# Optimization experiments

Hardware: AMD Instinct MI355X
Metric: run time of the kernel (lower is better)

## Reference

```python
import jax, jax.numpy as jnp
import numpy as np

N = 50000      # particles (nodes)
E = 300000     # contacts (directed edges), avg degree 6
H = 128        # hidden_features
L = 6          # num_hidden_layers
GF = 12        # graph (global) feature dim: domain(3)+t(1)+x_global(4)+domain_next(3)+t_next(1)
NG = 1         # number of graphs in batch
SP, SV, SW = 1e-3, 1e-3, 1e-2   # scale_position, scale_velocity, scale_angular_velocity
IN_EMB = GF + 1 + 6              # 19 : r + v + globals
IN_MSG = 2 * H + 3 + 6 + 2 + GF  # 279: h_i,h_j,dpos,dv,r_i,r_j,globals
IN_UPD = 2 * H + GF              # 268: h, aggregated message, globals


def _lin_params(key, fan_in, fan_out):
    k1, k2 = jax.random.split(key)
    s = 1.0 / np.sqrt(fan_in)
    W = jax.random.uniform(k1, (fan_in, fan_out), jnp.float32, -s, s)
    b = jax.random.uniform(k2, (fan_out,), jnp.float32, -s, s)
    return W, b


def setup_inputs() -> dict:
    key = jax.random.key(0)
    ks = jax.random.split(key, 40)
    inp = {}
    inp['v'] = jax.random.normal(ks[0], (N, 6), jnp.float32) * 0.01
    inp['pos'] = jax.random.uniform(ks[1], (N, 3), jnp.float32)
    inp['r'] = jax.random.uniform(ks[2], (N, 1), jnp.float32) * 0.05 + 0.01
    inp['domain'] = jnp.ones((3,), jnp.float32)
    inp['t'] = jnp.full((1,), 0.5, jnp.float32)
    inp['x_global'] = jax.random.normal(ks[3], (4,), jnp.float32)
    inp['domain_next'] = jnp.ones((3,), jnp.float32)
    inp['t_next'] = jnp.full((1,), 0.6, jnp.float32)
    inp['edge_index'] = jax.random.randint(ks[4], (2, E), 0, N, jnp.int32)
    inp['batch'] = jnp.zeros((N,), jnp.int32)
    inp['emb_W1'], inp['emb_b1'] = _lin_params(ks[5], IN_EMB, H)
    inp['emb_W2'], inp['emb_b2'] = _lin_params(ks[6], H, H)
    mw1, mb1, mw2, mb2, uw1, ub1, uw2, ub2 = ([] for _ in range(8))
    for l in range(L):
        W, b = _lin_params(ks[7 + l], IN_MSG, H); mw1.append(W); mb1.append(b)
        W, b = _lin_params(ks[13 + l], H, H);     mw2.append(W); mb2.append(b)
        W, b = _lin_params(ks[19 + l], IN_UPD, H); uw1.append(W); ub1.append(b)
        W, b = _lin_params(ks[25 + l], H, H);     uw2.append(W); ub2.append(b)
    inp['msg_W1'] = jnp.stack(mw1); inp['msg_b1'] = jnp.stack(mb1)
    inp['msg_W2'] = jnp.stack(mw2); inp['msg_b2'] = jnp.stack(mb2)
    inp['upd_W1'] = jnp.stack(uw1); inp['upd_b1'] = jnp.stack(ub1)
    inp['upd_W2'] = jnp.stack(uw2); inp['upd_b2'] = jnp.stack(ub2)
    inp['out_W1'], inp['out_b1'] = _lin_params(ks[31], H, H)
    inp['out_W2'], inp['out_b2'] = _lin_params(ks[32], H, 9)
    inp['mac_W1'], inp['mac_b1'] = _lin_params(ks[33], H, H)
    inp['mac_W2'], inp['mac_b2'] = _lin_params(ks[34], H, 3)
    return inp


def _instance_norm(h, batch):
    # per-graph, per-channel normalization over nodes (PyG InstanceNorm, affine=False)
    cnt = jax.ops.segment_sum(jnp.ones((h.shape[0],), h.dtype), batch, NG)[:, None]
    mean = jax.ops.segment_sum(h, batch, NG) / cnt
    d = h - mean[batch]
    var = jax.ops.segment_sum(d * d, batch, NG) / cnt
    return d / jnp.sqrt(var[batch] + 1e-5)


def reference(v, pos, r, domain, t, x_global, domain_next, t_next, edge_index, batch,
              emb_W1, emb_b1, emb_W2, emb_b2,
              msg_W1, msg_b1, msg_W2, msg_b2,
              upd_W1, upd_b1, upd_W2, upd_b2,
              out_W1, out_b1, out_W2, out_b2,
              mac_W1, mac_b1, mac_W2, mac_b2):
    gf = jnp.concatenate((domain, t, x_global, domain_next, t_next))   # [12]
    gfN = jnp.broadcast_to(gf, (v.shape[0], gf.shape[0]))
    node_features = jnp.concatenate((pos, v), axis=1)                  # [N,9]
    feat = jnp.concatenate((r, v, gfN), axis=1)                        # [N,19]
    h = jax.nn.relu(jax.nn.relu(feat @ emb_W1 + emb_b1) @ emb_W2 + emb_b2)
    src, dst = edge_index[0], edge_index[1]
    ones_e = jnp.ones((src.shape[0],), h.dtype)
    deg = jnp.maximum(jax.ops.segment_sum(ones_e, dst, v.shape[0]), 1.0)[:, None]
    gfE = jnp.broadcast_to(gf, (src.shape[0], gf.shape[0]))
    for l in range(L):
        dpos = pos[dst] - pos[src]
        dpos = dpos - domain * jnp.round(dpos / domain)                # periodic minimum image
        m_in = jnp.concatenate((h[dst], h[src], dpos, v[dst] - v[src], r[dst], r[src], gfE), axis=1)
        m = jax.nn.relu(jax.nn.relu(m_in @ msg_W1[l] + msg_b1[l]) @ msg_W2[l] + msg_b2[l])
        agg = jax.ops.segment_sum(m, dst, v.shape[0]) / deg            # mean aggregation
        u_in = jnp.concatenate((h, agg, gfN), axis=1)
        upd = jax.nn.relu(u_in @ upd_W1[l] + upd_b1[l]) @ upd_W2[l] + upd_b2[l]
        h = _instance_norm(h + upd, batch)                             # residual + InstanceNorm
    out = jax.nn.relu(h @ out_W1 + out_b1) @ out_W2 + out_b2           # [N,9]
    scaled = jnp.concatenate((SP * out[:, :3], SV * out[:, 3:6], SW * out[:, 6:]), axis=1)
    pred = scaled + node_features
    pred_x = jnp.remainder(pred[:, :3], domain_next)
    pred_v = pred[:, 3:]
    cnt = jax.ops.segment_sum(jnp.ones((h.shape[0],), h.dtype), batch, NG)[:, None]
    h_mean = jax.ops.segment_sum(h, batch, NG) / cnt                   # global mean pool
    pred_macro = (jax.nn.relu(h_mean @ mac_W1 + mac_b1) @ mac_W2 + mac_b2)[0]
    return (pred_x, pred_v, pred_macro)
```

## Files before the change

### kernel.cpp

```cpp
#include <hip/hip_runtime.h>

#define NNODES 50000
#define NEDGES 300000
#define NL 6
#define AP 132

typedef float f32x4 __attribute__((ext_vector_type(4)));
typedef short s16x8 __attribute__((ext_vector_type(8)));
typedef unsigned short u16x4 __attribute__((ext_vector_type(4)));

#define MFMA(A,B,C) __builtin_amdgcn_mfma_f32_16x16x32_bf16((A),(B),(C),0,0,0)

__device__ __forceinline__ unsigned short bf_hi(float x){
  unsigned u = __float_as_uint(x);
  u += 0x7fffu + ((u>>16)&1u);
  return (unsigned short)(u>>16);
}
__device__ __forceinline__ float bf_f(unsigned short s){
  return __uint_as_float(((unsigned)s)<<16);
}
__device__ __forceinline__ void split2(float x, unsigned short &h, unsigned short &l){
  h = bf_hi(x);
  l = bf_hi(x - bf_f(h));
}

__device__ __forceinline__ f32x4 mm3(s16x8 ah, s16x8 al, s16x8 bh, s16x8 bl, f32x4 c){
  c = MFMA(ah, bh, c);
  c = MFMA(ah, bl, c);
  c = MFMA(al, bh, c);
  return c;
}

__device__ __forceinline__ void pack_tile(const float* W, int K, const float* iv,
                                          unsigned short* dst, int kt, int nt, int lane){
  int col = nt*16 + (lane&15);
  int k0 = kt*32 + (lane>>4)*8;
  s16x8 hv, lv;
  #pragma unroll
  for(int j=0;j<8;j++){
    int k = k0 + j;
    float x = 0.f;
    if(k < K){
      x = W[(size_t)k*128 + col];
      if(iv) x *= iv[k];
    }
    unsigned short hh, ll; split2(x, hh, ll);
    hv[j] = (short)hh; lv[j] = (short)ll;
  }
  unsigned short* p = dst + ((size_t)((kt<<3)+nt)*64 + lane)*16;
  *(s16x8*)p = hv;
  *(s16x8*)(p+8) = lv;
}
__device__ __forceinline__ void ld_b(const unsigned short* P, int kt, int nt, int lane,
                                     s16x8 &bh, s16x8 &bl){
  const unsigned short* p = P + ((size_t)((kt<<3)+nt)*64 + lane)*16;
  bh = *(const s16x8*)p;
  bl = *(const s16x8*)(p+8);
}
__device__ __forceinline__ s16x8 ld_z(const unsigned short* z, int row, int kByte){
  return *(const s16x8*)((const char*)z + row*256 + (kByte ^ ((row&7)<<4)));
}
__device__ __forceinline__ void st_z(unsigned short* zH, unsigned short* zL, int row, int col, float x){
  unsigned short hh, ll; split2(x, hh, ll);
  int byte = row*256 + ((col*2) ^ ((row&7)<<4));
  *(unsigned short*)((char*)zH + byte) = hh;
  *(unsigned short*)((char*)zL + byte) = ll;
}
__device__ __forceinline__ s16x8 ld_t(const unsigned short* z, int row, int kByte){
  return *(const s16x8*)((const char*)z + row*64 + (kByte ^ ((row&3)<<4)));
}

__global__ void k_gf(const float* dom, const float* t, const float* xg,
                     const float* domn, const float* tn, float* gf){
  int i = threadIdx.x;
  if(i < 3)        gf[i]  = dom[i];
  else if(i == 3)  gf[3]  = t[0];
  else if(i < 8)   gf[i]  = xg[i-4];
  else if(i < 11)  gf[i]  = domn[i-8];
  else if(i == 11) gf[11] = tn[0];
}

__global__ void k_deg(const int* ei, float* deg){
  int e = blockIdx.x*blockDim.x + threadIdx.x;
  if(e < NEDGES) atomicAdd(&deg[ei[NEDGES + e]], 1.0f);
}

__global__ void k_histi(const int* ei, int* cnt){
  int e = blockIdx.x*blockDim.x + threadIdx.x;
  if(e < NEDGES) atomicAdd(&cnt[ei[NEDGES + e]], 1);
}

__global__ __launch_bounds__(1024) void k_scan(const int* cnt, int* off){
  __shared__ int buf[1024];
  __shared__ int carry;
  int t = threadIdx.x;
  if(t == 0) carry = 0;
  __syncthreads();
  for(int base = 0; base < NNODES; base += 1024){
    int i = base + t;
    int x = (i < NNODES) ? cnt[i] : 0;
    buf[t] = x;
    __syncthreads();
    for(int ofs = 1; ofs < 1024; ofs <<= 1){
      int y = (t >= ofs) ? buf[t-ofs] : 0;
      __syncthreads();
      buf[t] += y;
      __syncthreads();
    }
    if(i < NNODES) off[i] = carry + buf[t] - x;
    __syncthreads();
    if(t == 1023) carry += buf[1023];
    __syncthreads();
  }
  if(t == 0) off[NNODES] = carry;
}

__global__ void k_scatter(const int* ei, const int* off, int* cur, int* srcP, int* dstP){
  int e = blockIdx.x*blockDim.x + threadIdx.x;
  if(e < NEDGES){
    int s = ei[e], d = ei[NEDGES + e];
    int p = atomicAdd(&cur[d], 1);
    int ix = off[d] + p;
    srcP[ix] = s; dstP[ix] = d;
  }
}

__global__ void k_gfb(const float* gf, const float* mW1, const float* mB1, float* bb1){
  int i = blockIdx.x*256 + threadIdx.x;
  if(i < 768){
    int l = i >> 7, c = i & 127;
    float s = mB1[l*128 + c];
    #pragma unroll
    for(int j=0;j<12;j++) s = fmaf(gf[j], mW1[(size_t)l*35712 + (size_t)(267+j)*128 + c], s);
    bb1[i] = s;
  }
}

__global__ void k_gfb2(const float* gf, const float* mW1, const float* mB1,
                       const float* uW1, const float* uB1, float* bb1s, float* ub1s){
  int i = blockIdx.x*256 + threadIdx.x;
  if(i < 768){
    int l = i>>7, c = i&127;
    float s = mB1[l*128+c];
    #pragma unroll
    for(int j=0;j<12;j++) s = fmaf(gf[j], mW1[(size_t)l*35712 + (size_t)(267+j)*128 + c], s);
    bb1s[i] = s;
  } else if(i < 1536){
    int i2 = i-768, l = i2>>7, c = i2&127;
    float s = uB1[l*128+c];
    #pragma unroll
    for(int j=0;j<12;j++) s = fmaf(gf[j], uW1[(size_t)l*34304 + (size_t)(256+j)*128 + c], s);
    ub1s[i2] = s;
  }
}

__global__ void k_fold(const float* S, float* muiv, int l){
  int c = threadIdx.x;
  if(c >= 128) return;
  if(l == 0){ muiv[c] = 0.f; muiv[128+c] = 1.f; return; }
  float mean = S[c] * (1.0f/NNODES);
  float var  = S[128+c] * (1.0f/NNODES) - mean*mean;
  if(var < 0.f) var = 0.f;
  muiv[c] = mean;
  muiv[128+c] = rsqrtf(var + 1e-5f);
}

__global__ void k_dynbias(const float* muiv, const float* bb1s, const float* ub1s,
                          const float* msgW1l, const float* updW1l,
                          float* bb1d, float* ub1d){
  int c = threadIdx.x;
  if(blockIdx.x == 0){
    float s = bb1s[c];
    for(int k=0;k<128;k++){
      float f = muiv[k]*muiv[128+k];
      s -= f*(msgW1l[(size_t)k*128+c] + msgW1l[(size_t)(128+k)*128+c]);
    }
    bb1d[c] = s;
  } else {
    float s = ub1s[c];
    for(int k=0;k<128;k++) s -= muiv[k]*muiv[128+k]*updW1l[(size_t)k*128+c];
    ub1d[c] = s;
  }
}

__global__ void k_packAll(const float* msgW1, const float* msgW2,
                          const float* updW1, const float* updW2,
                          unsigned short* mPedge, unsigned short* mPw2,
                          unsigned short* uPagg, unsigned short* uPw2){
  int b = blockIdx.x, lane = threadIdx.x;
  if(b < 192){
    int l=b/32, t=b%32;
    pack_tile(msgW2 + (size_t)l*16384, 128, 0, mPw2 + (size_t)l*32768, t/8, t%8, lane);
  } else if(b < 384){
    int bb=b-192, l=bb/32, t=bb%32;
    pack_tile(updW1 + (size_t)l*34304 + 16384, 128, 0, uPagg + (size_t)l*32768, t/8, t%8, lane);
  } else if(b < 576){
    int bb=b-384, l=bb/32, t=bb%32;
    pack_tile(updW2 + (size_t)l*16384, 128, 0, uPw2 + (size_t)l*32768, t/8, t%8, lane);
  } else {
    int bb=b-576, l=bb/8, nt=bb%8;
    pack_tile(msgW1 + (size_t)l*35712 + 32768, 11, 0, mPedge + (size_t)l*8192, 0, nt, lane);
  }
}

__global__ void k_packDyn(const float* msgW1l, const float* updW1l, const float* muiv,
                          unsigned short* mPdst, unsigned short* mPsrc, unsigned short* uPh){
  int b = blockIdx.x, lane = threadIdx.x;
  const float* iv = muiv + 128;
  if(b < 32) pack_tile(msgW1l, 128, iv, mPdst, b>>3, b&7, lane);
  else if(b < 64){ int t=b-32; pack_tile(msgW1l + 16384, 128, iv, mPsrc, t>>3, t&7, lane); }
  else { int t=b-64; pack_tile(updW1l, 128, iv, uPh, t>>3, t&7, lane); }
}

__device__ __forceinline__ void fill_w(float* sW, const float* gW, int KC){
  for(int idx = threadIdx.x; idx < 32*32; idx += 256){
    int kk = idx >> 5, c4 = (idx & 31)*4;
    float4 w = make_float4(0.f,0.f,0.f,0.f);
    if(kk < KC) w = *(const float4*)(gW + (size_t)kk*128 + c4);
    *(float4*)(sW + kk*128 + c4) = w;
  }
}
__device__ __forceinline__ void gemm_chunk(const float* At, const float* sW,
                                           int KCp, int rg, int jc, float acc[4][4]){
  for(int kkg = 0; kkg < KCp; kkg += 4){
    float4 av[4];
    #pragma unroll
    for(int i=0;i<4;i++) av[i] = *(const float4*)(At + (rg*4+i)*AP + kkg);
    #pragma unroll
    for(int q=0;q<4;q++){
      float4 bq = *(const float4*)(sW + (kkg+q)*128 + 4*jc);
      #pragma unroll
      for(int i=0;i<4;i++){
        float aa = ((const float*)&av[i])[q];
        acc[i][0] = fmaf(aa, bq.x, acc[i][0]);
        acc[i][1] = fmaf(aa, bq.y, acc[i][1]);
        acc[i][2] = fmaf(aa, bq.z, acc[i][2]);
        acc[i][3] = fmaf(aa, bq.w, acc[i][3]);
      }
    }
  }
}
__device__ __forceinline__ void gemm_phase(const float* sA, float* sW, const float* gW,
                                           int K, int rg, int jc, float acc[4][4]){
  for(int k0 = 0; k0 < K; k0 += 32){
    int KC = (K - k0 < 32) ? (K - k0) : 32;
    __syncthreads();
    fill_w(sW, gW + (size_t)k0*128, KC);
    __syncthreads();
    gemm_chunk(sA + k0, sW, (KC+3)&~3, rg, jc, acc);
  }
}
__device__ __forceinline__ void init_bias(float acc[4][4], const float* b, int jc){
  float4 bb = *(const float4*)(b + 4*jc);
  #pragma unroll
  for(int i=0;i<4;i++){ acc[i][0]=bb.x; acc[i][1]=bb.y; acc[i][2]=bb.z; acc[i][3]=bb.w; }
}

__global__ __launch_bounds__(256) void k_embed(const float* r, const float* v, const float* gf,
    const float* W1, const float* b1, const float* W2, const float* b2, float* h,
    unsigned short* hPu){
  __shared__ __align__(16) float sA[32*AP];
  __shared__ __align__(16) float sW[32*128];
  __shared__ float sGf[12];
  int t = threadIdx.x, n0 = blockIdx.x*32;
  if(t < 12) sGf[t] = gf[t];
  __syncthreads();
  for(int idx = t; idx < 32*20; idx += 256){
    int row = idx/20, c = idx%20;
    int n = n0 + row; if(n >= NNODES) n = NNODES-1;
    float val;
    if(c == 0)      val = r[n];
    else if(c < 7)  val = v[(size_t)n*6 + (c-1)];
    else if(c < 19) val = sGf[c-7];
    else            val = 0.0f;
    sA[row*AP + c] = val;
  }
  int rg = t>>5, jc = t&31;
  float acc[4][4];
  init_bias(acc, b1, jc);
  gemm_phase(sA, sW, W1, 19, rg, jc, acc);
  __syncthreads();
  #pragma unroll
  for(int i=0;i<4;i++){
    float4 x = make_float4(fmaxf(acc[i][0],0.f), fmaxf(acc[i][1],0.f),
                           fmaxf(acc[i][2],0.f), fmaxf(acc[i][3],0.f));
    *(float4*)&sA[(rg*4+i)*AP + 4*jc] = x;
  }
  init_bias(acc, b2, jc);
  gemm_phase(sA, sW, W2, 128, rg, jc, acc);
  #pragma unroll
  for(int i=0;i<4;i++){
    int n = n0 + rg*4 + i;
    if(n < NNODES){
      float4 x = make_float4(fmaxf(acc[i][0],0.f), fmaxf(acc[i][1],0.f),
                             fmaxf(acc[i][2],0.f), fmaxf(acc[i][3],0.f));
      *(float4*)&h[(size_t)n*128 + 4*jc] = x;
      if(hPu){
        unsigned short h0,h1,h2,h3,l0,l1,l2,l3;
        split2(x.x,h0,l0); split2(x.y,h1,l1); split2(x.z,h2,l2); split2(x.w,h3,l3);
        u16x4 hv; hv[0]=h0; hv[1]=h1; hv[2]=h2; hv[3]=h3;
        u16x4 lv; lv[0]=l0; lv[1]=l1; lv[2]=l2; lv[3]=l3;
        *(u16x4*)&hPu[(size_t)n*256 + 4*jc] = hv;
        *(u16x4*)&hPu[(size_t)n*256 + 128 + 4*jc] = lv;
      }
    }
  }
}

__global__ __launch_bounds__(256) void k_msgM(const int* __restrict__ srcP, const int* __restrict__ dstP,
    const unsigned short* __restrict__ hPu,
    const float* __restrict__ pos, const float* __restrict__ v, const float* __restrict__ r,
    const float* __restrict__ dom,
    const unsigned short* __restrict__ mPdst, const unsigned short* __restrict__ mPsrc,
    const unsigned short* __restrict__ mPedge, const unsigned short* __restrict__ mPw2,
    const float* __restrict__ bb1d, const float* __restrict__ b2, float* __restrict__ agg)
{
  __shared__ __align__(16) unsigned short zBuf[8192];
  __shared__ __align__(16) unsigned short sTh[1024], sTl[1024];
  __shared__ int sSrc[32], sDst[32];
  __shared__ float sDom[3];
  unsigned short* zH = zBuf;
  unsigned short* zL = zBuf + 4096;
  int t = threadIdx.x, e0 = blockIdx.x*32;
  int w = t>>6, lane = t&63, lr = lane&15, g = lane>>4;
  int nt0 = w*2, nt1 = nt0+1;
  if(t < 32){ sSrc[t] = srcP[e0+t]; sDst[t] = dstP[e0+t]; }
  if(t >= 32 && t < 35) sDom[t-32] = dom[t-32];
  {
    s16x8 zz = {0,0,0,0,0,0,0,0};
    if(t < 128) ((s16x8*)sTh)[t] = zz;
    else ((s16x8*)sTl)[t-128] = zz;
  }
  __syncthreads();
  if(t < 32){
    int s = sSrc[t], d = sDst[t];
    float f[11];
    #pragma unroll
    for(int c=0;c<3;c++){
      float dp = pos[(size_t)d*3+c] - pos[(size_t)s*3+c];
      float dm = sDom[c];
      f[c] = dp - dm*rintf(dp/dm);
    }
    #pragma unroll
    for(int c=0;c<6;c++) f[3+c] = v[(size_t)d*6+c] - v[(size_t)s*6+c];
    f[9] = r[d]; f[10] = r[s];
    #pragma unroll
    for(int k=0;k<11;k++){
      unsigned short hh, ll; split2(f[k], hh, ll);
      int byte = t*64 + ((k*2) ^ ((t&3)<<4));
      *(unsigned short*)((char*)sTh + byte) = hh;
      *(unsigned short*)((char*)sTl + byte) = ll;
    }
  }
  float bias0 = bb1d[nt0*16+lr], bias1 = bb1d[nt1*16+lr];
  f32x4 a00 = {bias0,bias0,bias0,bias0};
  f32x4 a01 = {bias1,bias1,bias1,bias1};
  f32x4 a10 = a00, a11 = a01;
  __syncthreads();
  int d0 = sDst[lr], d1 = sDst[16+lr], s0 = sSrc[lr], s1 = sSrc[16+lr];
  const unsigned short* pd0 = hPu + (size_t)d0*256;
  const unsigned short* pd1 = hPu + (size_t)d1*256;
  const unsigned short* ps0 = hPu + (size_t)s0*256;
  const unsigned short* ps1 = hPu + (size_t)s1*256;
  int ko = g*8;
  #pragma unroll
  for(int kt=0;kt<4;kt++){
    int o = kt*32 + ko;
    s16x8 ah0 = *(const s16x8*)(pd0 + o), al0 = *(const s16x8*)(pd0 + 128 + o);
    s16x8 ah1 = *(const s16x8*)(pd1 + o), al1 = *(const s16x8*)(pd1 + 128 + o);
    s16x8 bh, bl;
    ld_b(mPdst, kt, nt0, lane, bh, bl);
    a00 = mm3(ah0, al0, bh, bl, a00);
    a10 = mm3(ah1, al1, bh, bl, a10);
    ld_b(mPdst, kt, nt1, lane, bh, bl);
    a01 = mm3(ah0, al0, bh, bl, a01);
    a11 = mm3(ah1, al1, bh, bl, a11);
    s16x8 ch0 = *(const s16x8*)(ps0 + o), cl0 = *(const s16x8*)(ps0 + 128 + o);
    s16x8 ch1 = *(const s16x8*)(ps1 + o), cl1 = *(const s16x8*)(ps1 + 128 + o);
    ld_b(mPsrc, kt, nt0, lane, bh, bl);
    a00 = mm3(ch0, cl0, bh, bl, a00);
    a10 = mm3(ch1, cl1, bh, bl, a10);
    ld_b(mPsrc, kt, nt1, lane, bh, bl);
    a01 = mm3(ch0, cl0, bh, bl, a01);
    a11 = mm3(ch1, cl1, bh, bl, a11);
  }
  {
    s16x8 th0 = ld_t(sTh, lr, ko*2),    tl0 = ld_t(sTl, lr, ko*2);
    s16x8 th1 = ld_t(sTh, 16+lr, ko*2), tl1 = ld_t(sTl, 16+lr, ko*2);
    s16x8 bh, bl;
    ld_b(mPedge, 0, nt0, lane, bh, bl);
    a00 = mm3(th0, tl0, bh, bl, a00);
    a10 = mm3(th1, tl1, bh, bl, a10);
    ld_b(mPedge, 0, nt1, lane, bh, bl);
    a01 = mm3(th0, tl0, bh, bl, a01);
    a11 = mm3(th1, tl1, bh, bl, a11);
  }
  #pragma unroll
  for(int i=0;i<4;i++){
    int r0 = g*4+i, r1 = 16+g*4+i;
    st_z(zH, zL, r0, nt0*16+lr, fmaxf(a00[i],0.f));
    st_z(zH, zL, r0, nt1*16+lr, fmaxf(a01[i],0.f));
    st_z(zH, zL, r1, nt0*16+lr, fmaxf(a10[i],0.f));
    st_z(zH, zL, r1, nt1*16+lr, fmaxf(a11[i],0.f));
  }
  __syncthreads();
  float c0 = b2[nt0*16+lr], c1 = b2[nt1*16+lr];
  f32x4 m00 = {c0,c0,c0,c0}, m01 = {c1,c1,c1,c1};
  f32x4 m10 = m00, m11 = m01;
  #pragma unroll
  for(int kt=0;kt<4;kt++){
    int kb = kt*64 + g*16;
    s16x8 ah0 = ld_z(zH, lr, kb),    al0 = ld_z(zL, lr, kb);
    s16x8 ah1 = ld_z(zH, 16+lr, kb), al1 = ld_z(zL, 16+lr, kb);
    s16x8 bh, bl;
    ld_b(mPw2, kt, nt0, lane, bh, bl);
    m00 = mm3(ah0, al0, bh, bl, m00);
    m10 = mm3(ah1, al1, bh, bl, m10);
    ld_b(mPw2, kt, nt1, lane, bh, bl);
    m01 = mm3(ah0, al0, bh, bl, m01);
    m11 = mm3(ah1, al1, bh, bl, m11);
  }
  __syncthreads();
  float* sM = (float*)zBuf;
  #pragma unroll
  for(int i=0;i<4;i++){
    int r0 = g*4+i, r1 = 16+g*4+i;
    sM[r0*128 + nt0*16+lr] = fmaxf(m00[i],0.f);
    sM[r0*128 + nt1*16+lr] = fmaxf(m01[i],0.f);
    sM[r1*128 + nt0*16+lr] = fmaxf(m10[i],0.f);
    sM[r1*128 + nt1*16+lr] = fmaxf(m11[i],0.f);
  }
  __syncthreads();
  int col = t & 127, half = t >> 7;
  int rbeg = half*16, rend = rbeg + 16;
  int cur = sDst[rbeg];
  float run = 0.f;
  for(int row = rbeg; row < rend; row++){
    run += sM[row*128 + col];
    int nxt = (row+1 < rend) ? sDst[row+1] : -1;
    if(nxt != cur){
      atomicAdd(&agg[(size_t)cur*128 + col], run);
      run = 0.f; cur = nxt;
    }
  }
}

__global__ __launch_bounds__(256) void k_updM(float* __restrict__ h, unsigned short* __restrict__ hPu,
    float* __restrict__ agg, const int* __restrict__ cnt, const float* __restrict__ muiv,
    const unsigned short* __restrict__ uPh, const unsigned short* __restrict__ uPagg,
    const unsigned short* __restrict__ uPw2,
    const float* __restrict__ ub1d, const float* __restrict__ b2, float* __restrict__ S)
{
  __shared__ __align__(16) unsigned short zBuf[8192];
  __shared__ __align__(16) float sH[32*AP];
  __shared__ float sRd[32];
  __shared__ float stS[512], stQ[512];
  unsigned short* zH = zBuf; unsigned short* zL = zBuf + 4096;
  int t = threadIdx.x, n0 = blockIdx.x*32;
  int w = t>>6, lane = t&63, lr = lane&15, g = lane>>4;
  int nt0 = w*2, nt1 = nt0+1;
  if(t < 32){
    int n = n0 + t; if(n >= NNODES) n = NNODES-1;
    sRd[t] = 1.0f / fmaxf((float)cnt[n], 1.0f);
  }
  __syncthreads();
  for(int idx = t; idx < 1024; idx += 256){
    int row = idx>>5, c4 = (idx&31)*4;
    int n = n0 + row; bool valid = (n < NNODES); if(!valid) n = NNODES-1;
    float4 hx = *(const float4*)&h[(size_t)n*128 + c4];
    *(float4*)&sH[row*AP + c4] = hx;
    float4 ax = *(const float4*)&agg[(size_t)n*128 + c4];
    float rd = sRd[row];
    ax.x*=rd; ax.y*=rd; ax.z*=rd; ax.w*=rd;
    unsigned short h0,h1,h2,h3,l0,l1,l2,l3;
    split2(ax.x,h0,l0); split2(ax.y,h1,l1); split2(ax.z,h2,l2); split2(ax.w,h3,l3);
    int byte = row*256 + ((c4*2) ^ ((row&7)<<4));
    u16x4 hv; hv[0]=h0; hv[1]=h1; hv[2]=h2; hv[3]=h3;
    u16x4 lv; lv[0]=l0; lv[1]=l1; lv[2]=l2; lv[3]=l3;
    *(u16x4*)((char*)zH + byte) = hv;
    *(u16x4*)((char*)zL + byte) = lv;
    if(valid) *(float4*)&agg[(size_t)n*128 + c4] = make_float4(0.f,0.f,0.f,0.f);
  }
  __syncthreads();
  float bias0 = ub1d[nt0*16+lr], bias1 = ub1d[nt1*16+lr];
  f32x4 a00 = {bias0,bias0,bias0,bias0};
  f32x4 a01 = {bias1,bias1,bias1,bias1};
  f32x4 a10 = a00, a11 = a01;
  int nA0 = n0+lr;    if(nA0 >= NNODES) nA0 = NNODES-1;
  int nA1 = n0+16+lr; if(nA1 >= NNODES) nA1 = NNODES-1;
  const unsigned short* ph0 = hPu + (size_t)nA0*256;
  const unsigned short* ph1 = hPu + (size_t)nA1*256;
  int ko = g*8;
  #pragma unroll
  for(int kt=0;kt<4;kt++){
    int o = kt*32 + ko;
    s16x8 ah0 = *(const s16x8*)(ph0 + o), al0 = *(const s16x8*)(ph0 + 128 + o);
    s16x8 ah1 = *(const s16x8*)(ph1 + o), al1 = *(const s16x8*)(ph1 + 128 + o);
    s16x8 bh, bl;
    ld_b(uPh, kt, nt0, lane, bh, bl);
    a00 = mm3(ah0, al0, bh, bl, a00);
    a10 = mm3(ah1, al1, bh, bl, a10);
    ld_b(uPh, kt, nt1, lane, bh, bl);
    a01 = mm3(ah0, al0, bh, bl, a01);
    a11 = mm3(ah1, al1, bh, bl, a11);
    int kb = kt*64 + g*16;
    s16x8 gh0 = ld_z(zH, lr, kb),    gl0 = ld_z(zL, lr, kb);
    s16x8 gh1 = ld_z(zH, 16+lr, kb), gl1 = ld_z(zL, 16+lr, kb);
    ld_b(uPagg, kt, nt0, lane, bh, bl);
    a00 = mm3(gh0, gl0, bh, bl, a00);
    a10 = mm3(gh1, gl1, bh, bl, a10);
    ld_b(uPagg, kt, nt1, lane, bh, bl);
    a01 = mm3(gh0, gl0, bh, bl, a01);
    a11 = mm3(gh1, gl1, bh, bl, a11);
  }
  __syncthreads();
  #pragma unroll
  for(int i=0;i<4;i++){
    int r0 = g*4+i, r1 = 16+g*4+i;
    st_z(zH, zL, r0, nt0*16+lr, fmaxf(a00[i],0.f));
    st_z(zH, zL, r0, nt1*16+lr, fmaxf(a01[i],0.f));
    st_z(zH, zL, r1, nt0*16+lr, fmaxf(a10[i],0.f));
    st_z(zH, zL, r1, nt1*16+lr, fmaxf(a11[i],0.f));
  }
  __syncthreads();
  float c0 = b2[nt0*16+lr], c1 = b2[nt1*16+lr];
  f32x4 m00 = {c0,c0,c0,c0}, m01 = {c1,c1,c1,c1};
  f32x4 m10 = m00, m11 = m01;
  #pragma unroll
  for(int kt=0;kt<4;kt++){
    int kb = kt*64 + g*16;
    s16x8 ah0 = ld_z(zH, lr, kb),    al0 = ld_z(zL, lr, kb);
    s16x8 ah1 = ld_z(zH, 16+lr, kb), al1 = ld_z(zL, 16+lr, kb);
    s16x8 bh, bl;
    ld_b(uPw2, kt, nt0, lane, bh, bl);
    m00 = mm3(ah0, al0, bh, bl, m00);
    m10 = mm3(ah1, al1, bh, bl, m10);
    ld_b(uPw2, kt, nt1, lane, bh, bl);
    m01 = mm3(ah0, al0, bh, bl, m01);
    m11 = mm3(ah1, al1, bh, bl, m11);
  }
  int col0 = nt0*16+lr, col1 = nt1*16+lr;
  float mu0 = muiv[col0], iv0 = muiv[128+col0];
  float mu1 = muiv[col1], iv1 = muiv[128+col1];
  float s0=0.f,q0=0.f,s1=0.f,q1=0.f;
  #pragma unroll
  for(int tm=0;tm<2;tm++){
    #pragma unroll
    for(int i=0;i<4;i++){
      int row = tm*16 + g*4 + i;
      int n = n0 + row;
      if(n < NNODES){
        float acc0 = (tm==0) ? m00[i] : m10[i];
        float acc1 = (tm==0) ? m01[i] : m11[i];
        float v0 = (sH[row*AP+col0]-mu0)*iv0 + acc0;
        float v1 = (sH[row*AP+col1]-mu1)*iv1 + acc1;
        h[(size_t)n*128+col0] = v0;
        h[(size_t)n*128+col1] = v1;
        unsigned short hh,ll;
        split2(v0,hh,ll); hPu[(size_t)n*256+col0]=hh; hPu[(size_t)n*256+128+col0]=ll;
        split2(v1,hh,ll); hPu[(size_t)n*256+col1]=hh; hPu[(size_t)n*256+128+col1]=ll;
        s0+=v0; q0+=v0*v0; s1+=v1; q1+=v1*v1;
      }
    }
  }
  stS[g*128+col0]=s0; stQ[g*128+col0]=q0;
  stS[g*128+col1]=s1; stQ[g*128+col1]=q1;
  __syncthreads();
  if(t < 128){
    float s = stS[t]+stS[128+t]+stS[256+t]+stS[384+t];
    float q = stQ[t]+stQ[128+t]+stQ[256+t]+stQ[384+t];
    atomicAdd(&S[t], s);
    atomicAdd(&S[128 + t], q);
  }
}

__global__ __launch_bounds__(256) void k_pre(const float* h, const float* W1, float* P){
  __shared__ __align__(16) float sA[32*AP];
  __shared__ __align__(16) float sW[32*128];
  int t = threadIdx.x, n0 = blockIdx.x*32;
  for(int idx = t; idx < 1024; idx += 256){
    int row = idx>>5, c4 = (idx&31)*4;
    int n = n0 + row; if(n >= NNODES) n = NNODES-1;
    *(float4*)&sA[row*AP + c4] = *(const float4*)&h[(size_t)n*128 + c4];
  }
  int rg = t>>5, jc = t&31;
  float acc[4][4];
  #pragma unroll
  for(int i=0;i<4;i++){ acc[i][0]=0.f; acc[i][1]=0.f; acc[i][2]=0.f; acc[i][3]=0.f; }
  gemm_phase(sA, sW, W1, 128, rg, jc, acc);
  #pragma unroll
  for(int i=0;i<4;i++){
    int n = n0 + rg*4 + i;
    if(n < NNODES)
      *(float4*)&P[(size_t)n*256 + 4*jc] = make_float4(acc[i][0],acc[i][1],acc[i][2],acc[i][3]);
  }
  #pragma unroll
  for(int i=0;i<4;i++){ acc[i][0]=0.f; acc[i][1]=0.f; acc[i][2]=0.f; acc[i][3]=0.f; }
  gemm_phase(sA, sW, W1 + (size_t)128*128, 128, rg, jc, acc);
  #pragma unroll
  for(int i=0;i<4;i++){
    int n = n0 + rg*4 + i;
    if(n < NNODES)
      *(float4*)&P[(size_t)n*256 + 128 + 4*jc] = make_float4(acc[i][0],acc[i][1],acc[i][2],acc[i][3]);
  }
}

__global__ __launch_bounds__(256) void k_msg2(const int* ei, const float* P,
    const float* pos, const float* v, const float* r, const float* dom,
    const float* W1, const float* W2, const float* bb1, const float* b2, float* agg){
  __shared__ __align__(16) float sM[32*AP];
  __shared__ __align__(16) float sW[32*128];
  __shared__ float sT[32*12];
  __shared__ float sB[128];
  __shared__ int sSrc[32], sDst[32];
  int t = threadIdx.x, e0 = blockIdx.x*32;
  if(t < 32){ sSrc[t] = ei[e0+t]; sDst[t] = ei[NEDGES + e0 + t]; }
  if(t >= 128) sB[t-128] = bb1[t-128];
  __syncthreads();
  for(int idx = t; idx < 352; idx += 256){
    int kk = idx>>5, c4 = (idx&31)*4;
    *(float4*)&sW[kk*128 + c4] = *(const float4*)&W1[(size_t)(256+kk)*128 + c4];
  }
  if(t < 32){
    int s = sSrc[t], d = sDst[t];
    #pragma unroll
    for(int c=0;c<3;c++){
      float dp = pos[(size_t)d*3+c] - pos[(size_t)s*3+c];
      float dm = dom[c];
      dp = dp - dm * rintf(dp/dm);
      sT[t*12 + c] = dp;
    }
    #pragma unroll
    for(int c=0;c<6;c++)
      sT[t*12 + 3 + c] = v[(size_t)d*6+c] - v[(size_t)s*6+c];
    sT[t*12 + 9]  = r[d];
    sT[t*12 + 10] = r[s];
    sT[t*12 + 11] = 0.0f;
  }
  for(int idx = t; idx < 1024; idx += 256){
    int row = idx>>5, c4 = (idx&31)*4;
    float4 pd = *(const float4*)&P[(size_t)sDst[row]*256 + c4];
    float4 ps = *(const float4*)&P[(size_t)sSrc[row]*256 + 128 + c4];
    float4 bb = *(const float4*)&sB[c4];
    *(float4*)&sM[row*AP + c4] = make_float4(bb.x+pd.x+ps.x, bb.y+pd.y+ps.y,
                                             bb.z+pd.z+ps.z, bb.w+pd.w+ps.w);
  }
  __syncthreads();
  int rg = t>>5, jc = t&31;
  float acc[4][4];
  #pragma unroll
  for(int i=0;i<4;i++)
    #pragma unroll
    for(int c=0;c<4;c++) acc[i][c] = sM[(rg*4+i)*AP + 4*jc + c];
  for(int k=0;k<11;k++){
    float4 b = *(const float4*)&sW[k*128 + 4*jc];
    #pragma unroll
    for(int i=0;i<4;i++){
      float a = sT[(rg*4+i)*12 + k];
      acc[i][0] = fmaf(a, b.x, acc[i][0]);
      acc[i][1] = fmaf(a, b.y, acc[i][1]);
      acc[i][2] = fmaf(a, b.z, acc[i][2]);
      acc[i][3] = fmaf(a, b.w, acc[i][3]);
    }
  }
  #pragma unroll
  for(int i=0;i<4;i++){
    float4 x = make_float4(fmaxf(acc[i][0],0.f), fmaxf(acc[i][1],0.f),
                           fmaxf(acc[i][2],0.f), fmaxf(acc[i][3],0.f));
    *(float4*)&sM[(rg*4+i)*AP + 4*jc] = x;
  }
  init_bias(acc, b2, jc);
  gemm_phase(sM, sW, W2, 128, rg, jc, acc);
  #pragma unroll
  for(int i=0;i<4;i++){
    int d = sDst[rg*4+i];
    #pragma unroll
    for(int c=0;c<4;c++)
      atomicAdd(&agg[(size_t)d*128 + 4*jc + c], fmaxf(acc[i][c], 0.0f));
  }
}

__global__ __launch_bounds__(256) void k_upd(float* h, const float* agg, const float* deg,
    const float* gf, const float* W1, const float* b1, const float* W2, const float* b2, int l){
  __shared__ __align__(16) float sA[32*AP];
  __shared__ __align__(16) float sW[32*128];
  __shared__ float sGf[12], sRd[32];
  int t = threadIdx.x, n0 = blockIdx.x*32;
  if(t < 12) sGf[t] = gf[t];
  if(t < 32){
    int n = n0 + t; if(n >= NNODES) n = NNODES-1;
    sRd[t] = 1.0f / fmaxf(deg[n], 1.0f);
  }
  __syncthreads();
  const float* Wl1 = W1 + (size_t)l*34304;
  const float* Wl2 = W2 + (size_t)l*16384;
  const float* bl1 = b1 + l*128;
  const float* bl2 = b2 + l*128;
  int rg = t>>5, jc = t&31;
  float acc[4][4];
  init_bias(acc, bl1, jc);
  for(int idx = t; idx < 1024; idx += 256){
    int row = idx>>5, c4 = (idx&31)*4;
    int n = n0 + row; if(n >= NNODES) n = NNODES-1;
    *(float4*)&sA[row*AP + c4] = *(const float4*)&h[(size_t)n*128 + c4];
  }
  gemm_phase(sA, sW, Wl1, 128, rg, jc, acc);
  __syncthreads();
  for(int idx = t; idx < 1024; idx += 256){
    int row = idx>>5, c4 = (idx&31)*4;
    int n = n0 + row; if(n >= NNODES) n = NNODES-1;
    float4 x = *(const float4*)&agg[(size_t)n*128 + c4];
    float rd = sRd[row];
    x.x*=rd; x.y*=rd; x.z*=rd; x.w*=rd;
    *(float4*)&sA[row*AP + c4] = x;
  }
  gemm_phase(sA, sW, Wl1 + (size_t)128*128, 128, rg, jc, acc);
  __syncthreads();
  if(t < 32){
    #pragma unroll
    for(int c=0;c<12;c++) sA[t*AP + c] = sGf[c];
  }
  gemm_phase(sA, sW, Wl1 + (size_t)256*128, 12, rg, jc, acc);
  __syncthreads();
  #pragma unroll
  for(int i=0;i<4;i++){
    float4 x = make_float4(fmaxf(acc[i][0],0.f), fmaxf(acc[i][1],0.f),
                           fmaxf(acc[i][2],0.f), fmaxf(acc[i][3],0.f));
    *(float4*)&sA[(rg*4+i)*AP + 4*jc] = x;
  }
  init_bias(acc, bl2, jc);
  gemm_phase(sA, sW, Wl2, 128, rg, jc, acc);
  #pragma unroll
  for(int i=0;i<4;i++){
    int n = n0 + rg*4 + i;
    if(n < NNODES){
      float4 x = *(const float4*)&h[(size_t)n*128 + 4*jc];
      x.x += acc[i][0]; x.y += acc[i][1]; x.z += acc[i][2]; x.w += acc[i][3];
      *(float4*)&h[(size_t)n*128 + 4*jc] = x;
    }
  }
}

__global__ __launch_bounds__(256) void k_stats(const float* h, float* sum, float* sq){
  int col = threadIdx.x & 127, half = threadIdx.x >> 7;
  float s = 0.f, q = 0.f;
  for(int n = blockIdx.x*2 + half; n < NNODES; n += gridDim.x*2){
    float x = h[(size_t)n*128 + col];
    s += x; q += x*x;
  }
  __shared__ float ls[256], lq[256];
  ls[threadIdx.x] = s; lq[threadIdx.x] = q;
  __syncthreads();
  if(half == 0){
    atomicAdd(&sum[col], ls[col] + ls[128+col]);
    atomicAdd(&sq[col],  lq[col] + lq[128+col]);
  }
}

__global__ void k_norm(float* h, const float* sum, const float* sq){
  size_t i = (size_t)blockIdx.x*256 + threadIdx.x;
  if(i < (size_t)NNODES*128){
    int col = i & 127;
    float mean = sum[col] * (1.0f/NNODES);
    float var  = sq[col] * (1.0f/NNODES) - mean*mean;
    if(var < 0.f) var = 0.f;
    h[i] = (h[i] - mean) * rsqrtf(var + 1e-5f);
  }
}

__global__ __launch_bounds__(256) void k_out(const float* h, const float* pos, const float* v,
    const float* domn, const float* W1, const float* b1, const float* W2, const float* b2,
    float* out){
  __shared__ __align__(16) float sA[32*AP];
  __shared__ __align__(16) float sW[32*128];
  __shared__ float sW2[128*9], sB2[9], sDn[3];
  int t = threadIdx.x, n0 = blockIdx.x*32;
  for(int idx = t; idx < 128*9; idx += 256) sW2[idx] = W2[idx];
  if(t < 9) sB2[t] = b2[t];
  if(t >= 16 && t < 19) sDn[t-16] = domn[t-16];
  for(int idx = t; idx < 1024; idx += 256){
    int row = idx>>5, c4 = (idx&31)*4;
    int n = n0 + row; if(n >= NNODES) n = NNODES-1;
    *(float4*)&sA[row*AP + c4] = *(const float4*)&h[(size_t)n*128 + c4];
  }
  int rg = t>>5, jc = t&31;
  float acc[4][4];
  init_bias(acc, b1, jc);
  gemm_phase(sA, sW, W1, 128, rg, jc, acc);
  __syncthreads();
  #pragma unroll
  for(int i=0;i<4;i++){
    float4 x = make_float4(fmaxf(acc[i][0],0.f), fmaxf(acc[i][1],0.f),
                           fmaxf(acc[i][2],0.f), fmaxf(acc[i][3],0.f));
    *(float4*)&sA[(rg*4+i)*AP + 4*jc] = x;
  }
  __syncthreads();
  for(int idx = t; idx < 32*9; idx += 256){
    int n = idx/9, c = idx%9;
    int gn = n0 + n;
    if(gn < NNODES){
      float s = sB2[c];
      for(int k=0;k<128;k++) s = fmaf(sA[n*AP + k], sW2[k*9 + c], s);
      if(c < 3){
        float p = 0.001f*s + pos[(size_t)gn*3 + c];
        float dn = sDn[c];
        p = p - floorf(p/dn)*dn;
        out[(size_t)gn*3 + c] = p;
      } else {
        float scale = (c < 6) ? 0.001f : 0.01f;
        float p = scale*s + v[(size_t)gn*6 + (c-3)];
        out[(size_t)150000 + (size_t)gn*6 + (c-3)] = p;
      }
    }
  }
}

__global__ __launch_bounds__(128) void k_macro(const float* sum, const float* W1,
    const float* b1, const float* W2, const float* b2, float* out){
  __shared__ float hm[128], t1[128];
  int t = threadIdx.x;
  hm[t] = sum[t] * (1.0f/NNODES);
  __syncthreads();
  float s = b1[t];
  for(int k=0;k<128;k++) s = fmaf(hm[k], W1[(size_t)k*128 + t], s);
  t1[t] = fmaxf(s, 0.0f);
  __syncthreads();
  if(t < 3){
    float o = b2[t];
    for(int k=0;k<128;k++) o = fmaf(t1[k], W2[(size_t)k*3 + t], o);
    out[450000 + t] = o;
  }
}

extern "C" void kernel_launch(void* const* d_in, const int* in_sizes, int n_in,
                              void* d_out, int out_size, void* d_ws, size_t ws_size,
                              hipStream_t stream){
  const float* v    = (const float*)d_in[0];
  const float* pos  = (const float*)d_in[1];
  const float* r    = (const float*)d_in[2];
  const float* dom  = (const float*)d_in[3];
  const float* tt   = (const float*)d_in[4];
  const float* xg   = (const float*)d_in[5];
  const float* domn = (const float*)d_in[6];
  const float* tn   = (const float*)d_in[7];
  const int*   ei   = (const int*)d_in[8];
  const float* embW1=(const float*)d_in[10]; const float* embB1=(const float*)d_in[11];
  const float* embW2=(const float*)d_in[12]; const float* embB2=(const float*)d_in[13];
  const float* msgW1=(const float*)d_in[14]; const float* msgB1=(const float*)d_in[15];
  const float* msgW2=(const float*)d_in[16]; const float* msgB2=(const float*)d_in[17];
  const float* updW1=(const float*)d_in[18]; const float* updB1=(const float*)d_in[19];
  const float* updW2=(const float*)d_in[20]; const float* updB2=(const float*)d_in[21];
  const float* outW1=(const float*)d_in[22]; const float* outB1=(const float*)d_in[23];
  const float* outW2=(const float*)d_in[24]; const float* outB2=(const float*)d_in[25];
  const float* macW1=(const float*)d_in[26]; const float* macB1=(const float*)d_in[27];
  const float* macW2=(const float*)d_in[28]; const float* macB2=(const float*)d_in[29];

  float* ws = (float*)d_ws;
  float* out = (float*)d_out;
  const bool mf = ws_size >= (size_t)105604292;

  if(mf){
    float* h    = ws;
    float* agg  = ws + (size_t)6400000;
    unsigned short* hPu = (unsigned short*)(ws + 12800000);
    float* Sb   = ws + (size_t)19200000;
    float* gf   = ws + (size_t)19201792;
    float* muiv = ws + (size_t)19201808;
    float* bb1s = ws + (size_t)19202064;
    float* ub1s = ws + (size_t)19202832;
    float* bb1d = ws + (size_t)19203600;
    float* ub1d = ws + (size_t)19203728;
    int* cnt  = (int*)(ws + 19203856);
    int* off  = (int*)(ws + 19253856);
    int* cur  = (int*)(ws + 19303857);
    int* srcP = (int*)(ws + 19353857);
    int* dstP = (int*)(ws + 19653857);
    unsigned short* mPdst  = (unsigned short*)(ws + 19953860);
    unsigned short* mPsrc  = (unsigned short*)(ws + 19970244);
    unsigned short* uPh    = (unsigned short*)(ws + 19986628);
    unsigned short* mPedge = (unsigned short*)(ws + 20003012);
    unsigned short* mPw2   = (unsigned short*)(ws + 20027588);
    unsigned short* uPagg  = (unsigned short*)(ws + 20125892);
    unsigned short* uPw2   = (unsigned short*)(ws + 20224196);

    k_gf<<<1, 64, 0, stream>>>(dom, tt, xg, domn, tn, gf);
    k_gfb2<<<6, 256, 0, stream>>>(gf, msgW1, msgB1, updW1, updB1, bb1s, ub1s);
    k_packAll<<<624, 64, 0, stream>>>(msgW1, msgW2, updW1, updW2, mPedge, mPw2, uPagg, uPw2);
    hipMemsetAsync(Sb, 0, 7*256*4, stream);
    hipMemsetAsync(agg, 0, (size_t)6400000*4, stream);
    hipMemsetAsync(cnt, 0, (size_t)NNODES*4, stream);
    hipMemsetAsync(cur, 0, (size_t)NNODES*4, stream);
    k_histi<<<(NEDGES+255)/256, 256, 0, stream>>>(ei, cnt);
    k_scan<<<1, 1024, 0, stream>>>(cnt, off);
    k_scatter<<<(NEDGES+255)/256, 256, 0, stream>>>(ei, off, cur, srcP, dstP);
    k_embed<<<(NNODES+31)/32, 256, 0, stream>>>(r, v, gf, embW1, embB1, embW2, embB2, h, hPu);
    for(int l = 0; l < NL; l++){
      k_fold<<<1, 128, 0, stream>>>((l > 0) ? (Sb + (l-1)*256) : Sb, muiv, l);
      k_dynbias<<<2, 128, 0, stream>>>(muiv, bb1s + l*128, ub1s + l*128,
          msgW1 + (size_t)l*35712, updW1 + (size_t)l*34304, bb1d, ub1d);
      k_packDyn<<<96, 64, 0, stream>>>(msgW1 + (size_t)l*35712, updW1 + (size_t)l*34304,
          muiv, mPdst, mPsrc, uPh);
      k_msgM<<<NEDGES/32, 256, 0, stream>>>(srcP, dstP, hPu, pos, v, r, dom,
          mPdst, mPsrc, mPedge + (size_t)l*8192, mPw2 + (size_t)l*32768,
          bb1d, msgB2 + l*128, agg);
      k_updM<<<(NNODES+31)/32, 256, 0, stream>>>(h, hPu, agg, cnt, muiv,
          uPh, uPagg + (size_t)l*32768, uPw2 + (size_t)l*32768,
          ub1d, updB2 + l*128, Sb + l*256);
    }
    k_norm<<<25000, 256, 0, stream>>>(h, Sb + 5*256, Sb + 5*256 + 128);
    k_stats<<<256, 256, 0, stream>>>(h, Sb + 6*256, Sb + 6*256 + 128);
    k_macro<<<1, 128, 0, stream>>>(Sb + 6*256, macW1, macB1, macW2, macB2, out);
    k_out<<<(NNODES+31)/32, 256, 0, stream>>>(h, pos, v, domn,
                                              outW1, outB1, outW2, outB2, out);
    return;
  }

  float* h   = ws;
  float* agg = ws + (size_t)6400000;
  float* P   = ws + (size_t)12800000;
  float* deg = ws + (size_t)25600000;
  float* gf  = ws + (size_t)25650016;
  float* sum = ws + (size_t)25650048;
  float* sq  = ws + (size_t)25650176;
  float* bb1 = ws + (size_t)25650304;

  k_gf<<<1, 64, 0, stream>>>(dom, tt, xg, domn, tn, gf);
  k_gfb<<<3, 256, 0, stream>>>(gf, msgW1, msgB1, bb1);
  hipMemsetAsync(deg, 0, (size_t)NNODES*4, stream);
  k_deg<<<(NEDGES+255)/256, 256, 0, stream>>>(ei, deg);
  k_embed<<<(NNODES+31)/32, 256, 0, stream>>>(r, v, gf, embW1, embB1, embW2, embB2, h,
                                              (unsigned short*)0);
  for(int l = 0; l < NL; l++){
    hipMemsetAsync(agg, 0, (size_t)6400000*4, stream);
    k_pre<<<(NNODES+31)/32, 256, 0, stream>>>(h, msgW1 + (size_t)l*35712, P);
    k_msg2<<<NEDGES/32, 256, 0, stream>>>(ei, P, pos, v, r, dom,
        msgW1 + (size_t)l*35712, msgW2 + (size_t)l*16384,
        bb1 + l*128, msgB2 + l*128, agg);
    k_upd<<<(NNODES+31)/32, 256, 0, stream>>>(h, agg, deg, gf,
        updW1, updB1, updW2, updB2, l);
    hipMemsetAsync(sum, 0, 128*4, stream);
    hipMemsetAsync(sq,  0, 128*4, stream);
    k_stats<<<256, 256, 0, stream>>>(h, sum, sq);
    k_norm<<<25000, 256, 0, stream>>>(h, sum, sq);
  }
  hipMemsetAsync(sum, 0, 128*4, stream);
  hipMemsetAsync(sq,  0, 128*4, stream);
  k_stats<<<256, 256, 0, stream>>>(h, sum, sq);
  k_macro<<<1, 128, 0, stream>>>(sum, macW1, macB1, macW2, macB2, out);
  k_out<<<(NNODES+31)/32, 256, 0, stream>>>(h, pos, v, domn,
                                            outW1, outB1, outW2, outB2, out);
}
```

Before: 1.908 ms.

## Process 64 edges per message block and swizzle block order across XCDs

The edge message kernel now handles 64 edges per block instead of 32. Each wave computes four 16-row tiles, so every packed weight fragment loaded from global memory is reused across twice as many edges. Block indices are remapped into eight contiguous groups, which likely improves L2 locality per XCD for sorted destinations. Invalid rows in the tail block are masked. In exchange, LDS use and register pressure roughly double, which may reduce occupancy.

```diff
diff --git a/kernel.cpp b/kernel.cpp
--- a/kernel.cpp
+++ b/kernel.cpp
@@ -307,7 +307,7 @@
   }
 }
 
-__global__ __launch_bounds__(256) void k_msgM(const int* __restrict__ srcP, const int* __restrict__ dstP,
+__global__ __launch_bounds__(256) void k_msgM2(const int* __restrict__ srcP, const int* __restrict__ dstP,
     const unsigned short* __restrict__ hPu,
     const float* __restrict__ pos, const float* __restrict__ v, const float* __restrict__ r,
     const float* __restrict__ dom,
@@ -315,24 +315,31 @@
     const unsigned short* __restrict__ mPedge, const unsigned short* __restrict__ mPw2,
     const float* __restrict__ bb1d, const float* __restrict__ b2, float* __restrict__ agg)
 {
-  __shared__ __align__(16) unsigned short zBuf[8192];
-  __shared__ __align__(16) unsigned short sTh[1024], sTl[1024];
-  __shared__ int sSrc[32], sDst[32];
+  __shared__ __align__(16) unsigned short zBuf[16384];
+  __shared__ __align__(16) unsigned short sTh[2048], sTl[2048];
+  __shared__ int sSrc[64], sDst[64];
   __shared__ float sDom[3];
   unsigned short* zH = zBuf;
-  unsigned short* zL = zBuf + 4096;
-  int t = threadIdx.x, e0 = blockIdx.x*32;
+  unsigned short* zL = zBuf + 8192;
+  int t = threadIdx.x;
+  int bid = blockIdx.x;
+  int swz = (bid & 7)*586 + (bid >> 3);
+  int e0 = swz*64;
+  int evalid = NEDGES - e0; if(evalid > 64) evalid = 64;
   int w = t>>6, lane = t&63, lr = lane&15, g = lane>>4;
   int nt0 = w*2, nt1 = nt0+1;
-  if(t < 32){ sSrc[t] = srcP[e0+t]; sDst[t] = dstP[e0+t]; }
-  if(t >= 32 && t < 35) sDom[t-32] = dom[t-32];
+  if(t < 64){
+    int ee = e0 + t; if(ee >= NEDGES) ee = NEDGES-1;
+    sSrc[t] = srcP[ee]; sDst[t] = dstP[ee];
+  }
+  if(t >= 64 && t < 67) sDom[t-64] = dom[t-64];
   {
     s16x8 zz = {0,0,0,0,0,0,0,0};
-    if(t < 128) ((s16x8*)sTh)[t] = zz;
-    else ((s16x8*)sTl)[t-128] = zz;
-  }
-  __syncthreads();
-  if(t < 32){
+    ((s16x8*)sTh)[t] = zz;
+    ((s16x8*)sTl)[t] = zz;
+  }
+  __syncthreads();
+  if(t < 64){
     int s = sSrc[t], d = sDst[t];
     float f[11];
     #pragma unroll
@@ -353,90 +360,115 @@
     }
   }
   float bias0 = bb1d[nt0*16+lr], bias1 = bb1d[nt1*16+lr];
-  f32x4 a00 = {bias0,bias0,bias0,bias0};
-  f32x4 a01 = {bias1,bias1,bias1,bias1};
-  f32x4 a10 = a00, a11 = a01;
-  __syncthreads();
-  int d0 = sDst[lr], d1 = sDst[16+lr], s0 = sSrc[lr], s1 = sSrc[16+lr];
-  const unsigned short* pd0 = hPu + (size_t)d0*256;
-  const unsigned short* pd1 = hPu + (size_t)d1*256;
-  const unsigned short* ps0 = hPu + (size_t)s0*256;
-  const unsigned short* ps1 = hPu + (size_t)s1*256;
+  f32x4 A0[4], A1[4];
+  #pragma unroll
+  for(int rt=0;rt<4;rt++){
+    f32x4 b0 = {bias0,bias0,bias0,bias0};
+    f32x4 b1v = {bias1,bias1,bias1,bias1};
+    A0[rt] = b0; A1[rt] = b1v;
+  }
+  __syncthreads();
+  const unsigned short* pd[4];
+  const unsigned short* ps[4];
+  #pragma unroll
+  for(int rt=0;rt<4;rt++){
+    pd[rt] = hPu + (size_t)sDst[rt*16+lr]*256;
+    ps[rt] = hPu + (size_t)sSrc[rt*16+lr]*256;
+  }
   int ko = g*8;
   #pragma unroll
   for(int kt=0;kt<4;kt++){
     int o = kt*32 + ko;
-    s16x8 ah0 = *(const s16x8*)(pd0 + o), al0 = *(const s16x8*)(pd0 + 128 + o);
-    s16x8 ah1 = *(const s16x8*)(pd1 + o), al1 = *(const s16x8*)(pd1 + 128 + o);
+    s16x8 DH[4], DL[4], SH[4], SL[4];
+    #pragma unroll
+    for(int rt=0;rt<4;rt++){
+      DH[rt] = *(const s16x8*)(pd[rt] + o);
+      DL[rt] = *(const s16x8*)(pd[rt] + 128 + o);
+      SH[rt] = *(const s16x8*)(ps[rt] + o);
+      SL[rt] = *(const s16x8*)(ps[rt] + 128 + o);
+    }
     s16x8 bh, bl;
     ld_b(mPdst, kt, nt0, lane, bh, bl);
-    a00 = mm3(ah0, al0, bh, bl, a00);
-    a10 = mm3(ah1, al1, bh, bl, a10);
+    #pragma unroll
+    for(int rt=0;rt<4;rt++) A0[rt] = mm3(DH[rt], DL[rt], bh, bl, A0[rt]);
     ld_b(mPdst, kt, nt1, lane, bh, bl);
-    a01 = mm3(ah0, al0, bh, bl, a01);
-    a11 = mm3(ah1, al1, bh, bl, a11);
-    s16x8 ch0 = *(const s16x8*)(ps0 + o), cl0 = *(const s16x8*)(ps0 + 128 + o);
-    s16x8 ch1 = *(const s16x8*)(ps1 + o), cl1 = *(const s16x8*)(ps1 + 128 + o);
+    #pragma unroll
+    for(int rt=0;rt<4;rt++) A1[rt] = mm3(DH[rt], DL[rt], bh, bl, A1[rt]);
     ld_b(mPsrc, kt, nt0, lane, bh, bl);
-    a00 = mm3(ch0, cl0, bh, bl, a00);
-    a10 = mm3(ch1, cl1, bh, bl, a10);
+    #pragma unroll
+    for(int rt=0;rt<4;rt++) A0[rt] = mm3(SH[rt], SL[rt], bh, bl, A0[rt]);
     ld_b(mPsrc, kt, nt1, lane, bh, bl);
-    a01 = mm3(ch0, cl0, bh, bl, a01);
-    a11 = mm3(ch1, cl1, bh, bl, a11);
+    #pragma unroll
+    for(int rt=0;rt<4;rt++) A1[rt] = mm3(SH[rt], SL[rt], bh, bl, A1[rt]);
   }
   {
-    s16x8 th0 = ld_t(sTh, lr, ko*2),    tl0 = ld_t(sTl, lr, ko*2);
-    s16x8 th1 = ld_t(sTh, 16+lr, ko*2), tl1 = ld_t(sTl, 16+lr, ko*2);
+    s16x8 TH[4], TL[4];
+    #pragma unroll
+    for(int rt=0;rt<4;rt++){
+      TH[rt] = ld_t(sTh, rt*16+lr, g*16);
+      TL[rt] = ld_t(sTl, rt*16+lr, g*16);
+    }
     s16x8 bh, bl;
     ld_b(mPedge, 0, nt0, lane, bh, bl);
-    a00 = mm3(th0, tl0, bh, bl, a00);
-    a10 = mm3(th1, tl1, bh, bl, a10);
+    #pragma unroll
+    for(int rt=0;rt<4;rt++) A0[rt] = mm3(TH[rt], TL[rt], bh, bl, A0[rt]);
     ld_b(mPedge, 0, nt1, lane, bh, bl);
-    a01 = mm3(th0, tl0, bh, bl, a01);
-    a11 = mm3(th1, tl1, bh, bl, a11);
-  }
-  #pragma unroll
-  for(int i=0;i<4;i++){
-    int r0 = g*4+i, r1 = 16+g*4+i;
-    st_z(zH, zL, r0, nt0*16+lr, fmaxf(a00[i],0.f));
-    st_z(zH, zL, r0, nt1*16+lr, fmaxf(a01[i],0.f));
-    st_z(zH, zL, r1, nt0*16+lr, fmaxf(a10[i],0.f));
-    st_z(zH, zL, r1, nt1*16+lr, fmaxf(a11[i],0.f));
+    #pragma unroll
+    for(int rt=0;rt<4;rt++) A1[rt] = mm3(TH[rt], TL[rt], bh, bl, A1[rt]);
+  }
+  #pragma unroll
+  for(int rt=0;rt<4;rt++){
+    #pragma unroll
+    for(int i=0;i<4;i++){
+      int row = rt*16 + g*4 + i;
+      st_z(zH, zL, row, nt0*16+lr, fmaxf(A0[rt][i],0.f));
+      st_z(zH, zL, row, nt1*16+lr, fmaxf(A1[rt][i],0.f));
+    }
   }
   __syncthreads();
   float c0 = b2[nt0*16+lr], c1 = b2[nt1*16+lr];
-  f32x4 m00 = {c0,c0,c0,c0}, m01 = {c1,c1,c1,c1};
-  f32x4 m10 = m00, m11 = m01;
+  f32x4 M0[4], M1[4];
+  #pragma unroll
+  for(int rt=0;rt<4;rt++){
+    f32x4 b0 = {c0,c0,c0,c0};
+    f32x4 b1v = {c1,c1,c1,c1};
+    M0[rt] = b0; M1[rt] = b1v;
+  }
   #pragma unroll
   for(int kt=0;kt<4;kt++){
     int kb = kt*64 + g*16;
-    s16x8 ah0 = ld_z(zH, lr, kb),    al0 = ld_z(zL, lr, kb);
-    s16x8 ah1 = ld_z(zH, 16+lr, kb), al1 = ld_z(zL, 16+lr, kb);
+    s16x8 ZHv[4], ZLv[4];
+    #pragma unroll
+    for(int rt=0;rt<4;rt++){
+      ZHv[rt] = ld_z(zH, rt*16+lr, kb);
+      ZLv[rt] = ld_z(zL, rt*16+lr, kb);
+    }
     s16x8 bh, bl;
     ld_b(mPw2, kt, nt0, lane, bh, bl);
-    m00 = mm3(ah0, al0, bh, bl, m00);
-    m10 = mm3(ah1, al1, bh, bl, m10);
+    #pragma unroll
+    for(int rt=0;rt<4;rt++) M0[rt] = mm3(ZHv[rt], ZLv[rt], bh, bl, M0[rt]);
     ld_b(mPw2, kt, nt1, lane, bh, bl);
-    m01 = mm3(ah0, al0, bh, bl, m01);
-    m11 = mm3(ah1, al1, bh, bl, m11);
+    #pragma unroll
+    for(int rt=0;rt<4;rt++) M1[rt] = mm3(ZHv[rt], ZLv[rt], bh, bl, M1[rt]);
   }
   __syncthreads();
   float* sM = (float*)zBuf;
   #pragma unroll
-  for(int i=0;i<4;i++){
-    int r0 = g*4+i, r1 = 16+g*4+i;
-    sM[r0*128 + nt0*16+lr] = fmaxf(m00[i],0.f);
-    sM[r0*128 + nt1*16+lr] = fmaxf(m01[i],0.f);
-    sM[r1*128 + nt0*16+lr] = fmaxf(m10[i],0.f);
-    sM[r1*128 + nt1*16+lr] = fmaxf(m11[i],0.f);
+  for(int rt=0;rt<4;rt++){
+    #pragma unroll
+    for(int i=0;i<4;i++){
+      int row = rt*16 + g*4 + i;
+      sM[row*128 + nt0*16+lr] = fmaxf(M0[rt][i],0.f);
+      sM[row*128 + nt1*16+lr] = fmaxf(M1[rt][i],0.f);
+    }
   }
   __syncthreads();
   int col = t & 127, half = t >> 7;
-  int rbeg = half*16, rend = rbeg + 16;
+  int rbeg = half*32, rend = rbeg + 32;
   int cur = sDst[rbeg];
   float run = 0.f;
   for(int row = rbeg; row < rend; row++){
-    run += sM[row*128 + col];
+    if(row < evalid) run += sM[row*128 + col];
     int nxt = (row+1 < rend) ? sDst[row+1] : -1;
     if(nxt != cur){
       atomicAdd(&agg[(size_t)cur*128 + col], run);
@@ -900,7 +932,7 @@
           msgW1 + (size_t)l*35712, updW1 + (size_t)l*34304, bb1d, ub1d);
       k_packDyn<<<96, 64, 0, stream>>>(msgW1 + (size_t)l*35712, updW1 + (size_t)l*34304,
           muiv, mPdst, mPsrc, uPh);
-      k_msgM<<<NEDGES/32, 256, 0, stream>>>(srcP, dstP, hPu, pos, v, r, dom,
+      k_msgM2<<<4688, 256, 0, stream>>>(srcP, dstP, hPu, pos, v, r, dom,
           mPdst, mPsrc, mPedge + (size_t)l*8192, mPw2 + (size_t)l*32768,
           bb1d, msgB2 + l*128, agg);
       k_updM<<<(NNODES+31)/32, 256, 0, stream>>>(h, hPu, agg, cnt, muiv,
```

Measured after the change: 1.861 ms. 2.4% less time.
